# Optimization experiments

Measured on AMD Instinct MI355X. Metric: run time of the kernel, lower is better.

The kernel has to match this reference:

```python
import jax, jax.numpy as jnp
import numpy as np

HEADS = 16
DIM_HEAD = 64
SCALE = DIM_HEAD ** -0.5
NEG = -jnp.finfo(jnp.float32).max


def setup_inputs() -> dict:
    key = jax.random.key(0)
    k1, k2, k3, k4, k5 = jax.random.split(key, 5)
    dim = 1024
    inner = HEADS * DIM_HEAD
    b, n = 2, 2048
    s = dim ** -0.5
    return {
        "x": jax.random.normal(k1, (b, n, dim), dtype=jnp.float32),
        "Wq": jax.random.normal(k2, (dim, inner), dtype=jnp.float32) * s,
        "Wk": jax.random.normal(k3, (dim, inner), dtype=jnp.float32) * s,
        "Wv": jax.random.normal(k4, (dim, inner), dtype=jnp.float32) * s,
        "Wo": jax.random.normal(k5, (inner, dim), dtype=jnp.float32) * s,
    }


def reference(x, Wq, Wk, Wv, Wo):
    b, n, _ = x.shape
    # project and split heads: b n (h d) -> b h n d
    def split(t):
        return t.reshape(b, n, HEADS, DIM_HEAD).transpose(0, 2, 1, 3)
    q = split(x @ Wq) * SCALE
    k = split(x @ Wk)
    v = split(x @ Wv)
    sim = jnp.einsum('bhid,bhjd->bhij', q, k)
    # causal mask: triu(j - i + 1) masked with -finfo.max
    causal = jnp.triu(jnp.ones((n, n), dtype=bool), k=1)
    sim = jnp.where(causal, NEG, sim)
    attn = jax.nn.softmax(sim, axis=-1)  # dropout p=0.0 -> identity
    out = jnp.einsum('bhij,bhjd->bhid', attn, v)
    out = out.transpose(0, 2, 1, 3).reshape(b, n, HEADS * DIM_HEAD)
    return out @ Wo
```

## Files before the change

kernel.cpp:

```cpp
#include <hip/hip_runtime.h>

#define NHEAD 16
#define DHEAD 64
#define SEQ 2048
#define DMODEL 1024
#define BATCH 2
#define QSCALE 0.1803368801111204f

typedef __bf16 bf16x8 __attribute__((ext_vector_type(8)));
typedef float f32x4 __attribute__((ext_vector_type(4)));
typedef float f32x16 __attribute__((ext_vector_type(16)));
typedef unsigned int u32x4 __attribute__((ext_vector_type(4)));

__device__ inline unsigned short f2bf(float f) {
  unsigned int u = __builtin_bit_cast(unsigned int, f);
  u = (u + 0x7FFFu + ((u >> 16) & 1u)) >> 16;
  return (unsigned short)u;
}

__device__ inline unsigned int cvtpk_bf16(float lo, float hi) {
  unsigned int r;
  asm("v_cvt_pk_bf16_f32 %0, %1, %2" : "=v"(r) : "v"(lo), "v"(hi));
  return r;
}

__device__ inline void pl32swap(unsigned int& a, unsigned int& b) {
  asm volatile("v_permlane32_swap_b32 %0, %1" : "+v"(a), "+v"(b));
}

__device__ inline float bflo(unsigned int u) { return __builtin_bit_cast(float, u << 16); }
__device__ inline float bfhi(unsigned int u) { return __builtin_bit_cast(float, u & 0xffff0000u); }

__global__ __launch_bounds__(256) void k_conv_x(const float* __restrict__ x,
                                                unsigned short* __restrict__ Af) {
  int blk = blockIdx.x;
  int R = blk >> 5, kt = blk & 31;
  int t = threadIdx.x;
  int i = t >> 6, lane = t & 63;
  int n = R * 64 + i * 16 + (lane & 15);
  int k = kt * 32 + (lane >> 4) * 8;
  const float* xp = x + (size_t)n * DMODEL + k;
  float4 v0 = *(const float4*)xp;
  float4 v1 = *(const float4*)(xp + 4);
  ushort4 lo, hi;
  lo.x = f2bf(v0.x); lo.y = f2bf(v0.y); lo.z = f2bf(v0.z); lo.w = f2bf(v0.w);
  hi.x = f2bf(v1.x); hi.y = f2bf(v1.y); hi.z = f2bf(v1.z); hi.w = f2bf(v1.w);
  size_t base = ((size_t)((R * 32 + kt) * 4 + i) * 64 + lane) * 8;
  *(ushort4*)&Af[base] = lo;
  *(ushort4*)&Af[base + 4] = hi;
}

__global__ __launch_bounds__(256) void k_trans_wf(const float* __restrict__ Wq, const float* __restrict__ Wk,
                                                  const float* __restrict__ Wv, const float* __restrict__ Wo,
                                                  unsigned short* __restrict__ Wqf, unsigned short* __restrict__ Wkf,
                                                  unsigned short* __restrict__ Wvf, unsigned short* __restrict__ Wof) {
  __shared__ float ts[32][65];
  int mat = blockIdx.z;
  const float* src = (mat == 0) ? Wq : (mat == 1) ? Wk : (mat == 2) ? Wv : Wo;
  unsigned short* dst = (mat == 0) ? Wqf : (mat == 1) ? Wkf : (mat == 2) ? Wvf : Wof;
  int cb = blockIdx.x, kt = blockIdx.y;
  int t = threadIdx.x;
  int row = t >> 3, seg = t & 7;
  const float* sp = src + (size_t)(kt * 32 + row) * DMODEL + cb * 64 + seg * 8;
  float4 u0 = *(const float4*)sp;
  float4 u1 = *(const float4*)(sp + 4);
  ts[row][seg * 8 + 0] = u0.x; ts[row][seg * 8 + 1] = u0.y;
  ts[row][seg * 8 + 2] = u0.z; ts[row][seg * 8 + 3] = u0.w;
  ts[row][seg * 8 + 4] = u1.x; ts[row][seg * 8 + 5] = u1.y;
  ts[row][seg * 8 + 6] = u1.z; ts[row][seg * 8 + 7] = u1.w;
  __syncthreads();
  int j = t >> 6, lane = t & 63;
  int c_l = j * 16 + (lane & 15);
  int kb = (lane >> 4) * 8;
  ushort4 lo, hi;
  lo.x = f2bf(ts[kb + 0][c_l]); lo.y = f2bf(ts[kb + 1][c_l]);
  lo.z = f2bf(ts[kb + 2][c_l]); lo.w = f2bf(ts[kb + 3][c_l]);
  hi.x = f2bf(ts[kb + 4][c_l]); hi.y = f2bf(ts[kb + 5][c_l]);
  hi.z = f2bf(ts[kb + 6][c_l]); hi.w = f2bf(ts[kb + 7][c_l]);
  size_t base = ((size_t)((cb * 32 + kt) * 4 + j) * 64 + lane) * 8;
  *(ushort4*)&dst[base] = lo;
  *(ushort4*)&dst[base + 4] = hi;
}

__global__ __launch_bounds__(128, 2) void k_gemm_qkv(const unsigned short* __restrict__ Af,
                                                     const unsigned short* __restrict__ Wqf,
                                                     const unsigned short* __restrict__ Wkf,
                                                     const unsigned short* __restrict__ Wvf,
                                                     unsigned short* __restrict__ Qf,
                                                     unsigned short* __restrict__ Kf,
                                                     unsigned short* __restrict__ Vf) {
  int id = blockIdx.x;
  int xcd = id & 7, lid = id >> 3;
  int rq = lid / 12, cw = lid % 12;
  int rho = (xcd >> 1) * 8 + rq;
  int wv = threadIdx.x >> 6;
  int R = rho * 2 + wv;
  int ct = (xcd & 1) * 12 + cw;
  int mat = ct >> 3, cb2 = ct & 7;
  const unsigned short* Bf = (mat == 0) ? Wqf : (mat == 1) ? Wkf : Wvf;
  int lane = threadIdx.x & 63;
  const unsigned short* Ap  = Af + (size_t)R * 65536 + lane * 8;
  const unsigned short* Bp0 = Bf + (size_t)(cb2 * 2) * 65536 + lane * 8;
  const unsigned short* Bp1 = Bp0 + 65536;

  f32x4 acc[4][8] = {};
  bf16x8 a0[4], a1[4], b0[8], b1[8];
#pragma unroll
  for (int i = 0; i < 4; i++) a0[i] = *(const bf16x8*)(Ap + i * 512);
#pragma unroll
  for (int j = 0; j < 4; j++) {
    b0[j]     = *(const bf16x8*)(Bp0 + j * 512);
    b0[4 + j] = *(const bf16x8*)(Bp1 + j * 512);
  }
#pragma unroll 1
  for (int kt = 0; kt < 32; kt += 2) {
    {
      const unsigned short* An = Ap + (kt + 1) * 2048;
      const unsigned short* Bn0 = Bp0 + (kt + 1) * 2048;
      const unsigned short* Bn1 = Bp1 + (kt + 1) * 2048;
#pragma unroll
      for (int i = 0; i < 4; i++) a1[i] = *(const bf16x8*)(An + i * 512);
#pragma unroll
      for (int j = 0; j < 4; j++) {
        b1[j]     = *(const bf16x8*)(Bn0 + j * 512);
        b1[4 + j] = *(const bf16x8*)(Bn1 + j * 512);
      }
    }
#pragma unroll
    for (int i = 0; i < 4; i++)
#pragma unroll
      for (int j = 0; j < 8; j++)
        acc[i][j] = __builtin_amdgcn_mfma_f32_16x16x32_bf16(a0[i], b0[j], acc[i][j], 0, 0, 0);
    if (kt + 2 < 32) {
      const unsigned short* An = Ap + (kt + 2) * 2048;
      const unsigned short* Bn0 = Bp0 + (kt + 2) * 2048;
      const unsigned short* Bn1 = Bp1 + (kt + 2) * 2048;
#pragma unroll
      for (int i = 0; i < 4; i++) a0[i] = *(const bf16x8*)(An + i * 512);
#pragma unroll
      for (int j = 0; j < 4; j++) {
        b0[j]     = *(const bf16x8*)(Bn0 + j * 512);
        b0[4 + j] = *(const bf16x8*)(Bn1 + j * 512);
      }
    }
#pragma unroll
    for (int i = 0; i < 4; i++)
#pragma unroll
      for (int j = 0; j < 8; j++)
        acc[i][j] = __builtin_amdgcn_mfma_f32_16x16x32_bf16(a1[i], b1[j], acc[i][j], 0, 0, 0);
  }

#pragma unroll
  for (int i = 0; i < 4; i++)
#pragma unroll
    for (int j = 0; j < 8; j++) {
      int n_g = R * 64 + i * 16 + ((lane >> 4) << 2);
      int c = cb2 * 128 + j * 16 + (lane & 15);
      int b = n_g >> 11, n0 = n_g & 2047;
      int h = c >> 6, d = c & 63;
      int bh = b * NHEAD + h;
      if (mat == 0) {
        size_t base = ((size_t)(bh * 64 + (n0 >> 5)) * 4 + (d >> 4)) * 512 +
                      (size_t)((((d >> 3) & 1) * 32 + (n0 & 31)) * 8 + (d & 7));
#pragma unroll
        for (int r = 0; r < 4; r++) Qf[base + 8 * r] = f2bf(acc[i][j][r] * QSCALE);
      } else if (mat == 1) {
        size_t base = ((size_t)(bh * 32 + (n0 >> 6)) * 8 + ((d >> 4) + 4 * ((n0 >> 5) & 1))) * 512 +
                      (size_t)((((d >> 3) & 1) * 32 + (n0 & 31)) * 8 + (d & 7));
#pragma unroll
        for (int r = 0; r < 4; r++) Kf[base + 8 * r] = f2bf(acc[i][j][r]);
      } else {
        size_t base = ((size_t)(bh * 32 + (n0 >> 6)) * 8 + (((n0 >> 4) & 3) + 4 * (d >> 5))) * 512 +
                      (size_t)((((n0 >> 3) & 1) * 32 + (d & 31)) * 8 + (n0 & 7));
        ushort4 o;
        o.x = f2bf(acc[i][j][0]); o.y = f2bf(acc[i][j][1]);
        o.z = f2bf(acc[i][j][2]); o.w = f2bf(acc[i][j][3]);
        *(ushort4*)&Vf[base] = o;
      }
    }
}

__global__ __launch_bounds__(64, 3) void k_attn_piece(const unsigned short* __restrict__ Qf,
                                                      const unsigned short* __restrict__ Kf,
                                                      const unsigned short* __restrict__ Vf,
                                                      unsigned short* __restrict__ Obf,
                                                      unsigned int* __restrict__ PartOb,
                                                      float* __restrict__ PartML) {
  int id = blockIdx.x;
  int xcd = id & 7, r = id >> 3;
  int bhl = r / 96, j = r % 96;
  int bh = xcd * 4 + bhl;
  int v = (j < 64) ? j : 127 - j;
  int nkFull = (v >> 1) + 1;
  int c0 = (j < 64) ? 0 : 16;
  int ce = (j < 64) ? ((nkFull < 16) ? nkFull : 16) : nkFull;
  int lane = threadIdx.x;
  int h = lane >> 5, ql = lane & 31;
  int qrow = v * 32 + ql;

  const unsigned short* Qp = Qf + (size_t)bh * 131072 + (size_t)v * 2048;
  const unsigned short* Kp = Kf + (size_t)bh * 131072;
  const unsigned short* Vp = Vf + (size_t)bh * 131072;

  bf16x8 qv[4];
#pragma unroll
  for (int ds = 0; ds < 4; ds++)
    qv[ds] = *(const bf16x8*)&Qp[ds * 512 + lane * 8];

  bf16x8 Kr[8], Vr[8];
  size_t cb0 = (size_t)c0 * 4096;
#pragma unroll
  for (int jj = 0; jj < 8; jj++) Kr[jj] = *(const bf16x8*)&Kp[cb0 + jj * 512 + lane * 8];
#pragma unroll
  for (int jj = 0; jj < 8; jj++) Vr[jj] = *(const bf16x8*)&Vp[cb0 + jj * 512 + lane * 8];

  f32x16 o0 = {}, o1 = {};
  float m_r = -3.0e38f, l_r = 0.0f;

#pragma unroll 1
  for (int kc = c0; kc < ce; ++kc) {
    f32x16 s0 = {}, s1 = {};
#pragma unroll
    for (int ds = 0; ds < 4; ds++) {
      s0 = __builtin_amdgcn_mfma_f32_32x32x16_bf16(Kr[ds], qv[ds], s0, 0, 0, 0);
      s1 = __builtin_amdgcn_mfma_f32_32x32x16_bf16(Kr[4 + ds], qv[ds], s1, 0, 0, 0);
    }
    bool pfn = (kc + 1 < ce);
    size_t nb = (size_t)(kc + 1) * 4096;
    if (pfn) {
#pragma unroll
      for (int jj2 = 0; jj2 < 8; jj2++) Kr[jj2] = *(const bf16x8*)&Kp[nb + jj2 * 512 + lane * 8];
    }
    int k0 = kc * 64;
    if (kc == nkFull - 1) {
#pragma unroll
      for (int r2 = 0; r2 < 16; r2++) {
        int kloc = (r2 & 3) + 8 * (r2 >> 2) + 4 * h;
        if (k0 + kloc > qrow) s0[r2] = -3.0e38f;
        if (k0 + 32 + kloc > qrow) s1[r2] = -3.0e38f;
      }
    }
    float t0[8], t1[8];
#pragma unroll
    for (int r2 = 0; r2 < 8; r2++) t0[r2] = fmaxf(s0[r2], s0[r2 + 8]);
#pragma unroll
    for (int r2 = 0; r2 < 8; r2++) t1[r2] = fmaxf(s1[r2], s1[r2 + 8]);
#pragma unroll
    for (int r2 = 0; r2 < 4; r2++) t0[r2] = fmaxf(fmaxf(t0[r2], t0[r2 + 4]), fmaxf(t1[r2], t1[r2 + 4]));
    float pm = fmaxf(fmaxf(t0[0], t0[1]), fmaxf(t0[2], t0[3]));
    pm = fmaxf(pm, __shfl_xor(pm, 32));
    bool grow = pm > m_r + 8.0f;
    float mnew = grow ? pm : m_r;
    float sf = grow ? __builtin_amdgcn_exp2f(m_r - mnew) : 1.0f;
    m_r = mnew;
    float rsum = 0.0f;
#pragma unroll
    for (int r2 = 0; r2 < 16; r2++) { s0[r2] = __builtin_amdgcn_exp2f(s0[r2] - m_r); rsum += s0[r2]; }
#pragma unroll
    for (int r2 = 0; r2 < 16; r2++) { s1[r2] = __builtin_amdgcn_exp2f(s1[r2] - m_r); rsum += s1[r2]; }
    l_r = l_r * sf + rsum;
    if (__ballot(grow)) {
#pragma unroll
      for (int r2 = 0; r2 < 16; r2++) { o0[r2] *= sf; o1[r2] *= sf; }
    }
    unsigned int pa0 = cvtpk_bf16(s0[0], s0[1]),   pa1 = cvtpk_bf16(s0[2], s0[3]);
    unsigned int pb0 = cvtpk_bf16(s0[4], s0[5]),   pb1 = cvtpk_bf16(s0[6], s0[7]);
    unsigned int pc0 = cvtpk_bf16(s0[8], s0[9]),   pc1 = cvtpk_bf16(s0[10], s0[11]);
    unsigned int pd0 = cvtpk_bf16(s0[12], s0[13]), pd1 = cvtpk_bf16(s0[14], s0[15]);
    unsigned int pe0 = cvtpk_bf16(s1[0], s1[1]),   pe1 = cvtpk_bf16(s1[2], s1[3]);
    unsigned int pf0 = cvtpk_bf16(s1[4], s1[5]),   pf1 = cvtpk_bf16(s1[6], s1[7]);
    unsigned int pg0 = cvtpk_bf16(s1[8], s1[9]),   pg1 = cvtpk_bf16(s1[10], s1[11]);
    unsigned int ph0 = cvtpk_bf16(s1[12], s1[13]), ph1 = cvtpk_bf16(s1[14], s1[15]);
    pl32swap(pa0, pb0); pl32swap(pa1, pb1);
    pl32swap(pc0, pd0); pl32swap(pc1, pd1);
    pl32swap(pe0, pf0); pl32swap(pe1, pf1);
    pl32swap(pg0, ph0); pl32swap(pg1, ph1);
    bf16x8 pfr[4];
    pfr[0] = __builtin_bit_cast(bf16x8, (u32x4){pa0, pa1, pb0, pb1});
    pfr[1] = __builtin_bit_cast(bf16x8, (u32x4){pc0, pc1, pd0, pd1});
    pfr[2] = __builtin_bit_cast(bf16x8, (u32x4){pe0, pe1, pf0, pf1});
    pfr[3] = __builtin_bit_cast(bf16x8, (u32x4){pg0, pg1, ph0, ph1});
#pragma unroll
    for (int ks = 0; ks < 4; ks++) {
      o0 = __builtin_amdgcn_mfma_f32_32x32x16_bf16(Vr[ks], pfr[ks], o0, 0, 0, 0);
      o1 = __builtin_amdgcn_mfma_f32_32x32x16_bf16(Vr[4 + ks], pfr[ks], o1, 0, 0, 0);
    }
    if (pfn) {
#pragma unroll
      for (int jj2 = 0; jj2 < 8; jj2++) Vr[jj2] = *(const bf16x8*)&Vp[nb + jj2 * 512 + lane * 8];
    }
  }

  float lt = l_r + __shfl_xor(l_r, 32);
  if (v < 32) {
    float rl = 1.0f / lt;
    int b = bh >> 4, hh = bh & 15;
    int Rg = b * 32 + (v >> 1);
    int ii = (v * 2 + (ql >> 4)) & 3;
    size_t base0 = ((size_t)(Rg * 32 + 2 * hh) * 4 + ii) * 512 + (size_t)((ql & 15) * 8 + 4 * h);
    size_t base1 = base0 + 2048;
#pragma unroll
    for (int rg = 0; rg < 4; rg++) {
      uint2 w0, w1;
      w0.x = cvtpk_bf16(o0[4 * rg] * rl, o0[4 * rg + 1] * rl);
      w0.y = cvtpk_bf16(o0[4 * rg + 2] * rl, o0[4 * rg + 3] * rl);
      w1.x = cvtpk_bf16(o1[4 * rg] * rl, o1[4 * rg + 1] * rl);
      w1.y = cvtpk_bf16(o1[4 * rg + 2] * rl, o1[4 * rg + 3] * rl);
      *(uint2*)&Obf[base0 + rg * 128] = w0;
      *(uint2*)&Obf[base1 + rg * 128] = w1;
    }
  } else {
    int pidx = (((bh << 5) + (v - 32)) << 1) + ((j >= 64) ? 1 : 0);
    unsigned int* po = PartOb + (size_t)pidx * 1024 + lane * 16;
#pragma unroll
    for (int rg = 0; rg < 4; rg++) {
      po[rg * 2]     = cvtpk_bf16(o0[4 * rg], o0[4 * rg + 1]);
      po[rg * 2 + 1] = cvtpk_bf16(o0[4 * rg + 2], o0[4 * rg + 3]);
      po[8 + rg * 2]     = cvtpk_bf16(o1[4 * rg], o1[4 * rg + 1]);
      po[8 + rg * 2 + 1] = cvtpk_bf16(o1[4 * rg + 2], o1[4 * rg + 3]);
    }
    PartML[(size_t)pidx * 128 + lane * 2]     = m_r;
    PartML[(size_t)pidx * 128 + lane * 2 + 1] = lt;
  }
}

__global__ __launch_bounds__(64, 4) void k_attn_merge(const unsigned int* __restrict__ PartOb,
                                                      const float* __restrict__ PartML,
                                                      unsigned short* __restrict__ Obf) {
  int t = blockIdx.x;
  int bh = t >> 5, v = 32 + (t & 31);
  int lane = threadIdx.x, h = lane >> 5, ql = lane & 31;
  int p0i = ((bh << 5) + (v - 32)) << 1;
  const unsigned int* q0 = PartOb + (size_t)p0i * 1024 + lane * 16;
  const unsigned int* q1 = q0 + 1024;
  float m1 = PartML[(size_t)p0i * 128 + lane * 2];
  float l1 = PartML[(size_t)p0i * 128 + lane * 2 + 1];
  float m2 = PartML[(size_t)(p0i + 1) * 128 + lane * 2];
  float l2 = PartML[(size_t)(p0i + 1) * 128 + lane * 2 + 1];
  float m = fmaxf(m1, m2);
  float w1 = __builtin_amdgcn_exp2f(m1 - m);
  float w2 = __builtin_amdgcn_exp2f(m2 - m);
  float rl = 1.0f / (w1 * l1 + w2 * l2);
  float W1 = w1 * rl, W2 = w2 * rl;
  unsigned int ow[16];
#pragma unroll
  for (int w = 0; w < 16; w++) {
    unsigned int a = q0[w], c = q1[w];
    float lo = W1 * bflo(a) + W2 * bflo(c);
    float hi = W1 * bfhi(a) + W2 * bfhi(c);
    ow[w] = cvtpk_bf16(lo, hi);
  }
  int b = bh >> 4, hh = bh & 15;
  int Rg = b * 32 + (v >> 1);
  int ii = (v * 2 + (ql >> 4)) & 3;
  size_t base0 = ((size_t)(Rg * 32 + 2 * hh) * 4 + ii) * 512 + (size_t)((ql & 15) * 8 + 4 * h);
  size_t base1 = base0 + 2048;
#pragma unroll
  for (int rg = 0; rg < 4; rg++) {
    uint2 w0, w1u;
    w0.x  = ow[2 * rg];     w0.y  = ow[2 * rg + 1];
    w1u.x = ow[8 + 2 * rg]; w1u.y = ow[8 + 2 * rg + 1];
    *(uint2*)&Obf[base0 + rg * 128] = w0;
    *(uint2*)&Obf[base1 + rg * 128] = w1u;
  }
}

__global__ __launch_bounds__(64, 2) void k_gemm_out(const unsigned short* __restrict__ Obf,
                                                    const unsigned short* __restrict__ Wof,
                                                    float* __restrict__ out) {
  int id = blockIdx.x;
  int xcd = id & 7, lid = id >> 3;
  int rg8 = lid >> 4, cb = lid & 15;
  int R = xcd * 8 + rg8;
  int lane = threadIdx.x;
  const unsigned short* Ap = Obf + (size_t)R * 65536 + lane * 8;
  const unsigned short* Bp = Wof + (size_t)cb * 65536 + lane * 8;

  f32x4 acc[4][4] = {};
  bf16x8 a0[4], b0[4], a1[4], b1[4];
#pragma unroll
  for (int i = 0; i < 4; i++) {
    a0[i] = *(const bf16x8*)(Ap + i * 512);
    b0[i] = *(const bf16x8*)(Bp + i * 512);
  }
#pragma unroll 1
  for (int kt = 0; kt < 32; kt += 2) {
    {
      const unsigned short* An = Ap + (kt + 1) * 2048;
      const unsigned short* Bn = Bp + (kt + 1) * 2048;
#pragma unroll
      for (int i = 0; i < 4; i++) {
        a1[i] = *(const bf16x8*)(An + i * 512);
        b1[i] = *(const bf16x8*)(Bn + i * 512);
      }
    }
#pragma unroll
    for (int i = 0; i < 4; i++)
#pragma unroll
      for (int j = 0; j < 4; j++)
        acc[i][j] = __builtin_amdgcn_mfma_f32_16x16x32_bf16(a0[i], b0[j], acc[i][j], 0, 0, 0);
    if (kt + 2 < 32) {
      const unsigned short* An = Ap + (kt + 2) * 2048;
      const unsigned short* Bn = Bp + (kt + 2) * 2048;
#pragma unroll
      for (int i = 0; i < 4; i++) {
        a0[i] = *(const bf16x8*)(An + i * 512);
        b0[i] = *(const bf16x8*)(Bn + i * 512);
      }
    }
#pragma unroll
    for (int i = 0; i < 4; i++)
#pragma unroll
      for (int j = 0; j < 4; j++)
        acc[i][j] = __builtin_amdgcn_mfma_f32_16x16x32_bf16(a1[i], b1[j], acc[i][j], 0, 0, 0);
  }

#pragma unroll
  for (int i = 0; i < 4; i++)
#pragma unroll
    for (int j = 0; j < 4; j++) {
      int n_g = R * 64 + i * 16 + ((lane >> 4) << 2);
      int c = cb * 64 + j * 16 + (lane & 15);
#pragma unroll
      for (int r = 0; r < 4; r++)
        out[(size_t)(n_g + r) * DMODEL + c] = acc[i][j][r];
    }
}

extern "C" void kernel_launch(void* const* d_in, const int* in_sizes, int n_in,
                              void* d_out, int out_size, void* d_ws, size_t ws_size,
                              hipStream_t stream) {
  const float* x  = (const float*)d_in[0];
  const float* Wq = (const float*)d_in[1];
  const float* Wk = (const float*)d_in[2];
  const float* Wv = (const float*)d_in[3];
  const float* Wo = (const float*)d_in[4];
  float* out = (float*)d_out;
  char* ws = (char*)d_ws;
  unsigned short* Af  = (unsigned short*)(ws);
  unsigned short* Wqf = (unsigned short*)(ws + (8ull << 20));
  unsigned short* Wkf = (unsigned short*)(ws + (10ull << 20));
  unsigned short* Wvf = (unsigned short*)(ws + (12ull << 20));
  unsigned short* Wof = (unsigned short*)(ws + (14ull << 20));
  unsigned short* Qf  = (unsigned short*)(ws + (16ull << 20));
  unsigned short* Kf  = (unsigned short*)(ws + (24ull << 20));
  unsigned short* Vf  = (unsigned short*)(ws + (32ull << 20));
  unsigned short* Obf = (unsigned short*)(ws + (40ull << 20));
  unsigned int* PartOb = (unsigned int*)(ws);
  float* PartML = (float*)(ws + (8ull << 20));

  k_conv_x<<<dim3(2048), dim3(256), 0, stream>>>(x, Af);
  k_trans_wf<<<dim3(16, 32, 4), dim3(256), 0, stream>>>(Wq, Wk, Wv, Wo, Wqf, Wkf, Wvf, Wof);
  k_gemm_qkv<<<dim3(768), dim3(128), 0, stream>>>(Af, Wqf, Wkf, Wvf, Qf, Kf, Vf);
  k_attn_piece<<<dim3(3072), dim3(64), 0, stream>>>(Qf, Kf, Vf, Obf, PartOb, PartML);
  k_attn_merge<<<dim3(1024), dim3(64), 0, stream>>>(PartOb, PartML, Obf);
  k_gemm_out<<<dim3(1024), dim3(64), 0, stream>>>(Obf, Wof, out);
}
```

Measured before the change: 113.8 us.

## Rebalance causal attention split into 12-chunk pieces, fuse prep kernels, raise occupancy

Causal attention work is redistributed: query tiles are split into 1, 2 or 3 pieces of at most 12 key chunks, scheduled heaviest-first, and the merge kernel combines up to three partials. The two preprocessing kernels (x conversion and weight transposition) are merged into one launch, attention launch bounds go from 3 to 4 waves per SIMD, and the softmax row sum becomes a tree reduction. The aim is better load balance and less launch overhead, at the cost of more partial-result traffic, a three-way merge, and possible register pressure from the higher occupancy target.

```diff
diff --git a/kernel.cpp b/kernel.cpp
--- a/kernel.cpp
+++ b/kernel.cpp
@@ -31,55 +31,56 @@
 __device__ inline float bflo(unsigned int u) { return __builtin_bit_cast(float, u << 16); }
 __device__ inline float bfhi(unsigned int u) { return __builtin_bit_cast(float, u & 0xffff0000u); }
 
-__global__ __launch_bounds__(256) void k_conv_x(const float* __restrict__ x,
-                                                unsigned short* __restrict__ Af) {
-  int blk = blockIdx.x;
-  int R = blk >> 5, kt = blk & 31;
-  int t = threadIdx.x;
-  int i = t >> 6, lane = t & 63;
-  int n = R * 64 + i * 16 + (lane & 15);
-  int k = kt * 32 + (lane >> 4) * 8;
-  const float* xp = x + (size_t)n * DMODEL + k;
-  float4 v0 = *(const float4*)xp;
-  float4 v1 = *(const float4*)(xp + 4);
-  ushort4 lo, hi;
-  lo.x = f2bf(v0.x); lo.y = f2bf(v0.y); lo.z = f2bf(v0.z); lo.w = f2bf(v0.w);
-  hi.x = f2bf(v1.x); hi.y = f2bf(v1.y); hi.z = f2bf(v1.z); hi.w = f2bf(v1.w);
-  size_t base = ((size_t)((R * 32 + kt) * 4 + i) * 64 + lane) * 8;
-  *(ushort4*)&Af[base] = lo;
-  *(ushort4*)&Af[base + 4] = hi;
-}
-
-__global__ __launch_bounds__(256) void k_trans_wf(const float* __restrict__ Wq, const float* __restrict__ Wk,
-                                                  const float* __restrict__ Wv, const float* __restrict__ Wo,
-                                                  unsigned short* __restrict__ Wqf, unsigned short* __restrict__ Wkf,
-                                                  unsigned short* __restrict__ Wvf, unsigned short* __restrict__ Wof) {
+__global__ __launch_bounds__(256) void k_pre(const float* __restrict__ x,
+                                             const float* __restrict__ Wq, const float* __restrict__ Wk,
+                                             const float* __restrict__ Wv, const float* __restrict__ Wo,
+                                             unsigned short* __restrict__ Af,
+                                             unsigned short* __restrict__ Wqf, unsigned short* __restrict__ Wkf,
+                                             unsigned short* __restrict__ Wvf, unsigned short* __restrict__ Wof) {
   __shared__ float ts[32][65];
-  int mat = blockIdx.z;
-  const float* src = (mat == 0) ? Wq : (mat == 1) ? Wk : (mat == 2) ? Wv : Wo;
-  unsigned short* dst = (mat == 0) ? Wqf : (mat == 1) ? Wkf : (mat == 2) ? Wvf : Wof;
-  int cb = blockIdx.x, kt = blockIdx.y;
-  int t = threadIdx.x;
-  int row = t >> 3, seg = t & 7;
-  const float* sp = src + (size_t)(kt * 32 + row) * DMODEL + cb * 64 + seg * 8;
-  float4 u0 = *(const float4*)sp;
-  float4 u1 = *(const float4*)(sp + 4);
-  ts[row][seg * 8 + 0] = u0.x; ts[row][seg * 8 + 1] = u0.y;
-  ts[row][seg * 8 + 2] = u0.z; ts[row][seg * 8 + 3] = u0.w;
-  ts[row][seg * 8 + 4] = u1.x; ts[row][seg * 8 + 5] = u1.y;
-  ts[row][seg * 8 + 6] = u1.z; ts[row][seg * 8 + 7] = u1.w;
-  __syncthreads();
-  int j = t >> 6, lane = t & 63;
-  int c_l = j * 16 + (lane & 15);
-  int kb = (lane >> 4) * 8;
-  ushort4 lo, hi;
-  lo.x = f2bf(ts[kb + 0][c_l]); lo.y = f2bf(ts[kb + 1][c_l]);
-  lo.z = f2bf(ts[kb + 2][c_l]); lo.w = f2bf(ts[kb + 3][c_l]);
-  hi.x = f2bf(ts[kb + 4][c_l]); hi.y = f2bf(ts[kb + 5][c_l]);
-  hi.z = f2bf(ts[kb + 6][c_l]); hi.w = f2bf(ts[kb + 7][c_l]);
-  size_t base = ((size_t)((cb * 32 + kt) * 4 + j) * 64 + lane) * 8;
-  *(ushort4*)&dst[base] = lo;
-  *(ushort4*)&dst[base + 4] = hi;
+  if (blockIdx.x < 2048) {
+    int blk = blockIdx.x;
+    int R = blk >> 5, kt = blk & 31;
+    int t = threadIdx.x;
+    int i = t >> 6, lane = t & 63;
+    int n = R * 64 + i * 16 + (lane & 15);
+    int k = kt * 32 + (lane >> 4) * 8;
+    const float* xp = x + (size_t)n * DMODEL + k;
+    float4 v0 = *(const float4*)xp;
+    float4 v1 = *(const float4*)(xp + 4);
+    ushort4 lo, hi;
+    lo.x = f2bf(v0.x); lo.y = f2bf(v0.y); lo.z = f2bf(v0.z); lo.w = f2bf(v0.w);
+    hi.x = f2bf(v1.x); hi.y = f2bf(v1.y); hi.z = f2bf(v1.z); hi.w = f2bf(v1.w);
+    size_t base = ((size_t)((R * 32 + kt) * 4 + i) * 64 + lane) * 8;
+    *(ushort4*)&Af[base] = lo;
+    *(ushort4*)&Af[base + 4] = hi;
+  } else {
+    int blk2 = blockIdx.x - 2048;
+    int cb = blk2 & 15, kt = (blk2 >> 4) & 31, mat = blk2 >> 9;
+    const float* src = (mat == 0) ? Wq : (mat == 1) ? Wk : (mat == 2) ? Wv : Wo;
+    unsigned short* dst = (mat == 0) ? Wqf : (mat == 1) ? Wkf : (mat == 2) ? Wvf : Wof;
+    int t = threadIdx.x;
+    int row = t >> 3, seg = t & 7;
+    const float* sp = src + (size_t)(kt * 32 + row) * DMODEL + cb * 64 + seg * 8;
+    float4 u0 = *(const float4*)sp;
+    float4 u1 = *(const float4*)(sp + 4);
+    ts[row][seg * 8 + 0] = u0.x; ts[row][seg * 8 + 1] = u0.y;
+    ts[row][seg * 8 + 2] = u0.z; ts[row][seg * 8 + 3] = u0.w;
+    ts[row][seg * 8 + 4] = u1.x; ts[row][seg * 8 + 5] = u1.y;
+    ts[row][seg * 8 + 6] = u1.z; ts[row][seg * 8 + 7] = u1.w;
+    __syncthreads();
+    int j = t >> 6, lane = t & 63;
+    int c_l = j * 16 + (lane & 15);
+    int kb = (lane >> 4) * 8;
+    ushort4 lo, hi;
+    lo.x = f2bf(ts[kb + 0][c_l]); lo.y = f2bf(ts[kb + 1][c_l]);
+    lo.z = f2bf(ts[kb + 2][c_l]); lo.w = f2bf(ts[kb + 3][c_l]);
+    hi.x = f2bf(ts[kb + 4][c_l]); hi.y = f2bf(ts[kb + 5][c_l]);
+    hi.z = f2bf(ts[kb + 6][c_l]); hi.w = f2bf(ts[kb + 7][c_l]);
+    size_t base = ((size_t)((cb * 32 + kt) * 4 + j) * 64 + lane) * 8;
+    *(ushort4*)&dst[base] = lo;
+    *(ushort4*)&dst[base + 4] = hi;
+  }
 }
 
 __global__ __launch_bounds__(128, 2) void k_gemm_qkv(const unsigned short* __restrict__ Af,
@@ -180,7 +181,7 @@
     }
 }
 
-__global__ __launch_bounds__(64, 3) void k_attn_piece(const unsigned short* __restrict__ Qf,
+__global__ __launch_bounds__(64, 4) void k_attn_piece(const unsigned short* __restrict__ Qf,
                                                       const unsigned short* __restrict__ Kf,
                                                       const unsigned short* __restrict__ Vf,
                                                       unsigned short* __restrict__ Obf,
@@ -188,12 +189,16 @@
                                                       float* __restrict__ PartML) {
   int id = blockIdx.x;
   int xcd = id & 7, r = id >> 3;
-  int bhl = r / 96, j = r % 96;
+  int bhl = r & 3, qi = r >> 2;
+  int q = 119 - qi;
   int bh = xcd * 4 + bhl;
-  int v = (j < 64) ? j : 127 - j;
+  int v, pi, np;
+  if (q < 24)      { v = q;                         pi = 0;              np = 1; }
+  else if (q < 72) { int t = q - 24; v = 24 + (t >> 1); pi = t & 1;      np = 2; }
+  else             { int t = q - 72; int t3 = t / 3; v = 48 + t3; pi = t - t3 * 3; np = 3; }
   int nkFull = (v >> 1) + 1;
-  int c0 = (j < 64) ? 0 : 16;
-  int ce = (j < 64) ? ((nkFull < 16) ? nkFull : 16) : nkFull;
+  int c0 = pi * 12;
+  int ce = c0 + 12; if (ce > nkFull) ce = nkFull;
   int lane = threadIdx.x;
   int h = lane >> 5, ql = lane & 31;
   int qrow = v * 32 + ql;
@@ -253,11 +258,19 @@
     float mnew = grow ? pm : m_r;
     float sf = grow ? __builtin_amdgcn_exp2f(m_r - mnew) : 1.0f;
     m_r = mnew;
-    float rsum = 0.0f;
-#pragma unroll
-    for (int r2 = 0; r2 < 16; r2++) { s0[r2] = __builtin_amdgcn_exp2f(s0[r2] - m_r); rsum += s0[r2]; }
-#pragma unroll
-    for (int r2 = 0; r2 < 16; r2++) { s1[r2] = __builtin_amdgcn_exp2f(s1[r2] - m_r); rsum += s1[r2]; }
+#pragma unroll
+    for (int r2 = 0; r2 < 16; r2++) s0[r2] = __builtin_amdgcn_exp2f(s0[r2] - m_r);
+#pragma unroll
+    for (int r2 = 0; r2 < 16; r2++) s1[r2] = __builtin_amdgcn_exp2f(s1[r2] - m_r);
+    float u0 = (s0[0] + s0[1]) + (s0[2] + s0[3]);
+    float u1 = (s0[4] + s0[5]) + (s0[6] + s0[7]);
+    float u2 = (s0[8] + s0[9]) + (s0[10] + s0[11]);
+    float u3 = (s0[12] + s0[13]) + (s0[14] + s0[15]);
+    float u4 = (s1[0] + s1[1]) + (s1[2] + s1[3]);
+    float u5 = (s1[4] + s1[5]) + (s1[6] + s1[7]);
+    float u6 = (s1[8] + s1[9]) + (s1[10] + s1[11]);
+    float u7 = (s1[12] + s1[13]) + (s1[14] + s1[15]);
+    float rsum = ((u0 + u1) + (u2 + u3)) + ((u4 + u5) + (u6 + u7));
     l_r = l_r * sf + rsum;
     if (__ballot(grow)) {
 #pragma unroll
@@ -292,7 +305,7 @@
   }
 
   float lt = l_r + __shfl_xor(l_r, 32);
-  if (v < 32) {
+  if (np == 1) {
     float rl = 1.0f / lt;
     int b = bh >> 4, hh = bh & 15;
     int Rg = b * 32 + (v >> 1);
@@ -310,7 +323,8 @@
       *(uint2*)&Obf[base1 + rg * 128] = w1;
     }
   } else {
-    int pidx = (((bh << 5) + (v - 32)) << 1) + ((j >= 64) ? 1 : 0);
+    int tbase = (v < 48) ? (v - 24) * 2 : 48 + (v - 48) * 3;
+    int pidx = bh * 96 + tbase + pi;
     unsigned int* po = PartOb + (size_t)pidx * 1024 + lane * 16;
 #pragma unroll
     for (int rg = 0; rg < 4; rg++) {
@@ -328,27 +342,38 @@
                                                       const float* __restrict__ PartML,
                                                       unsigned short* __restrict__ Obf) {
   int t = blockIdx.x;
-  int bh = t >> 5, v = 32 + (t & 31);
+  int bh = t / 40, w = t % 40;
+  int v, np, tbase;
+  if (w < 24) { v = 24 + w; np = 2; tbase = w * 2; }
+  else        { v = 48 + (w - 24); np = 3; tbase = 48 + (w - 24) * 3; }
+  int slot0 = bh * 96 + tbase;
   int lane = threadIdx.x, h = lane >> 5, ql = lane & 31;
-  int p0i = ((bh << 5) + (v - 32)) << 1;
-  const unsigned int* q0 = PartOb + (size_t)p0i * 1024 + lane * 16;
+  const unsigned int* q0 = PartOb + (size_t)slot0 * 1024 + lane * 16;
   const unsigned int* q1 = q0 + 1024;
-  float m1 = PartML[(size_t)p0i * 128 + lane * 2];
-  float l1 = PartML[(size_t)p0i * 128 + lane * 2 + 1];
-  float m2 = PartML[(size_t)(p0i + 1) * 128 + lane * 2];
-  float l2 = PartML[(size_t)(p0i + 1) * 128 + lane * 2 + 1];
-  float m = fmaxf(m1, m2);
+  const unsigned int* q2 = q0 + 2048;
+  float m0 = PartML[(size_t)slot0 * 128 + lane * 2];
+  float l0 = PartML[(size_t)slot0 * 128 + lane * 2 + 1];
+  float m1 = PartML[(size_t)(slot0 + 1) * 128 + lane * 2];
+  float l1 = PartML[(size_t)(slot0 + 1) * 128 + lane * 2 + 1];
+  float m2 = -3.0e38f, l2 = 0.0f;
+  if (np == 3) {
+    m2 = PartML[(size_t)(slot0 + 2) * 128 + lane * 2];
+    l2 = PartML[(size_t)(slot0 + 2) * 128 + lane * 2 + 1];
+  }
+  float m = fmaxf(fmaxf(m0, m1), m2);
+  float w0 = __builtin_amdgcn_exp2f(m0 - m);
   float w1 = __builtin_amdgcn_exp2f(m1 - m);
-  float w2 = __builtin_amdgcn_exp2f(m2 - m);
-  float rl = 1.0f / (w1 * l1 + w2 * l2);
-  float W1 = w1 * rl, W2 = w2 * rl;
+  float w2 = (np == 3) ? __builtin_amdgcn_exp2f(m2 - m) : 0.0f;
+  float rl = 1.0f / (w0 * l0 + w1 * l1 + w2 * l2);
+  float W0 = w0 * rl, W1 = w1 * rl, W2 = w2 * rl;
   unsigned int ow[16];
 #pragma unroll
-  for (int w = 0; w < 16; w++) {
-    unsigned int a = q0[w], c = q1[w];
-    float lo = W1 * bflo(a) + W2 * bflo(c);
-    float hi = W1 * bfhi(a) + W2 * bfhi(c);
-    ow[w] = cvtpk_bf16(lo, hi);
+  for (int wd = 0; wd < 16; wd++) {
+    unsigned int a = q0[wd], c = q1[wd];
+    unsigned int e = (np == 3) ? q2[wd] : 0u;
+    float lo = W0 * bflo(a) + W1 * bflo(c) + W2 * bflo(e);
+    float hi = W0 * bfhi(a) + W1 * bfhi(c) + W2 * bfhi(e);
+    ow[wd] = cvtpk_bf16(lo, hi);
   }
   int b = bh >> 4, hh = bh & 15;
   int Rg = b * 32 + (v >> 1);
@@ -357,11 +382,11 @@
   size_t base1 = base0 + 2048;
 #pragma unroll
   for (int rg = 0; rg < 4; rg++) {
-    uint2 w0, w1u;
-    w0.x  = ow[2 * rg];     w0.y  = ow[2 * rg + 1];
-    w1u.x = ow[8 + 2 * rg]; w1u.y = ow[8 + 2 * rg + 1];
-    *(uint2*)&Obf[base0 + rg * 128] = w0;
-    *(uint2*)&Obf[base1 + rg * 128] = w1u;
+    uint2 wa, wb;
+    wa.x = ow[2 * rg];     wa.y = ow[2 * rg + 1];
+    wb.x = ow[8 + 2 * rg]; wb.y = ow[8 + 2 * rg + 1];
+    *(uint2*)&Obf[base0 + rg * 128] = wa;
+    *(uint2*)&Obf[base1 + rg * 128] = wb;
   }
 }
 
@@ -447,12 +472,11 @@
   unsigned short* Vf  = (unsigned short*)(ws + (32ull << 20));
   unsigned short* Obf = (unsigned short*)(ws + (40ull << 20));
   unsigned int* PartOb = (unsigned int*)(ws);
-  float* PartML = (float*)(ws + (8ull << 20));
-
-  k_conv_x<<<dim3(2048), dim3(256), 0, stream>>>(x, Af);
-  k_trans_wf<<<dim3(16, 32, 4), dim3(256), 0, stream>>>(Wq, Wk, Wv, Wo, Wqf, Wkf, Wvf, Wof);
+  float* PartML = (float*)(ws + (12ull << 20));
+
+  k_pre<<<dim3(4096), dim3(256), 0, stream>>>(x, Wq, Wk, Wv, Wo, Af, Wqf, Wkf, Wvf, Wof);
   k_gemm_qkv<<<dim3(768), dim3(128), 0, stream>>>(Af, Wqf, Wkf, Wvf, Qf, Kf, Vf);
-  k_attn_piece<<<dim3(3072), dim3(64), 0, stream>>>(Qf, Kf, Vf, Obf, PartOb, PartML);
-  k_attn_merge<<<dim3(1024), dim3(64), 0, stream>>>(PartOb, PartML, Obf);
+  k_attn_piece<<<dim3(3840), dim3(64), 0, stream>>>(Qf, Kf, Vf, Obf, PartOb, PartML);
+  k_attn_merge<<<dim3(1280), dim3(64), 0, stream>>>(PartOb, PartML, Obf);
   k_gemm_out<<<dim3(1024), dim3(64), 0, stream>>>(Obf, Wof, out);
 }
```

Measured after the change: 199.8 us. 1.76x slower.
